# Kernel optimization log

Hardware: AMD Instinct MI355X
Metric: run time of the kernel (lower is better)

Reference implementation:

```python
import jax, jax.numpy as jnp
import numpy as np

N, E, K, F_IN, H = 50000, 640000, 3, 128, 128


def setup_inputs() -> dict:
    key = jax.random.key(0)
    ks = jax.random.split(key, 14)
    s = 0.05
    return {
        "x": jax.random.normal(ks[0], (N, F_IN), jnp.float32),
        "edge_index": jax.random.randint(ks[1], (2, E), 0, N, dtype=jnp.int32),
        "edge_weight": jax.random.uniform(ks[2], (E,), jnp.float32, minval=0.1, maxval=1.0),
        "W_x": jax.random.normal(ks[3], (4, F_IN, H), jnp.float32) * s,   # dense input weights (i,f,c,o)
        "w_c": jax.random.normal(ks[4], (3, H), jnp.float32) * s,         # peephole weights (i,f,o)
        "b": jax.random.normal(ks[5], (4, H), jnp.float32) * s,           # gate biases (i,f,c,o)
        "theta": jax.random.normal(ks[6], (4, K, H, H), jnp.float32) * s, # ChebConv weights per gate
        "theta_b": jax.random.normal(ks[7], (4, H), jnp.float32) * s,     # ChebConv biases per gate
        "gcn_w": jax.random.normal(ks[8], (H, H), jnp.float32) * s,
        "gcn_b": jnp.zeros((H,), jnp.float32),
        "bn_gamma": jnp.ones((H,), jnp.float32),
        "bn_beta": jnp.zeros((H,), jnp.float32),
        "bn_mean": jax.random.normal(ks[9], (H,), jnp.float32) * 0.1,
        "bn_var": jax.random.uniform(ks[10], (H,), jnp.float32, minval=0.5, maxval=1.5),
        "lin_w": jax.random.normal(ks[11], (H, 1), jnp.float32) * s,
        "lin_b": jnp.zeros((1,), jnp.float32),
    }


def reference(x, edge_index, edge_weight, W_x, w_c, b, theta, theta_b, gcn_w, gcn_b, bn_gamma, bn_beta, bn_mean, bn_var, lin_w, lin_b):
    n = x.shape[0]
    src, dst = edge_index[0], edge_index[1]

    # --- ChebConv normalization (sym, lambda_max=2): L_hat = -D^{-1/2} A D^{-1/2}, zero diagonal ---
    deg = jnp.zeros((n,), x.dtype).at[src].add(edge_weight)
    safe = jnp.where(deg > 0, deg, 1.0)
    dis = jnp.where(deg > 0, jax.lax.rsqrt(safe), 0.0)
    lw = -dis[src] * edge_weight * dis[dst]  # per-edge scaled-Laplacian weight

    def prop(h):  # out[i] = sum_{edges j->i} lw * h[j]
        return jnp.zeros_like(h).at[dst].add(lw[:, None] * h[src])

    def cheb(h, th, tb):  # sum_k T_k(L_hat) h @ theta_k + bias, Chebyshev recurrence
        Tx0, out = h, h @ th[0]
        Tx1 = prop(h)
        out = out + Tx1 @ th[1]
        for k in range(2, K):
            Tx2 = 2.0 * prop(Tx1) - Tx0
            out = out + Tx2 @ th[k]
            Tx0, Tx1 = Tx1, Tx2
        return out + tb

    # --- GCLSTM with H = C = 0 (module passes no initial state) ---
    Hs = jnp.zeros((n, W_x.shape[2]), x.dtype)
    Cs = jnp.zeros_like(Hs)
    I = jax.nn.sigmoid(x @ W_x[0] + cheb(Hs, theta[0], theta_b[0]) + w_c[0] * Cs + b[0])
    Fg = jax.nn.sigmoid(x @ W_x[1] + cheb(Hs, theta[1], theta_b[1]) + w_c[1] * Cs + b[1])
    T = jnp.tanh(x @ W_x[2] + cheb(Hs, theta[2], theta_b[2]) + b[2])
    Cs = Fg * Cs + I * T
    O = jax.nn.sigmoid(x @ W_x[3] + cheb(Hs, theta[3], theta_b[3]) + w_c[2] * Cs + b[3])
    Hs = O * jnp.tanh(Cs)

    # --- GCNConv(H) with unit edge weights + added self-loops ---
    h = Hs @ gcn_w
    deg_g = jnp.ones((n,), x.dtype).at[dst].add(jnp.ones((edge_index.shape[1],), x.dtype))
    dg = jax.lax.rsqrt(deg_g)
    g = jnp.zeros_like(h).at[dst].add((dg[src] * dg[dst])[:, None] * h[src]) + (dg * dg)[:, None] * h + gcn_b

    g = jax.nn.relu(g)
    g = bn_gamma * (g - bn_mean) * jax.lax.rsqrt(bn_var + 1e-5) + bn_beta  # BatchNorm1d (eval)
    return g @ lin_w + lin_b  # Dropout = identity in eval
```

## Files before the change

kernel.cpp:

```cpp
#include <hip/hip_runtime.h>
#include <hip/hip_bf16.h>

#define NN 50000
#define NE 640000
#define NP 196
#define CAP 64
#define NGB 782
#define NFB 625

typedef unsigned short ushort_t;
typedef unsigned int uint_t;
typedef __attribute__((ext_vector_type(8))) short bf16x8;
typedef __attribute__((ext_vector_type(4))) float f32x4;

__device__ __forceinline__ float b2f(ushort_t u) {
    union { uint_t u; float f; } v; v.u = ((uint_t)u) << 16; return v.f;
}
__device__ __forceinline__ ushort_t f2b(float f) {
    union { float f; uint_t u; } v; v.f = f;
    uint_t u = v.u;
    uint_t r = u + 0x7fffu + ((u >> 16) & 1u);
    return (ushort_t)(r >> 16);
}
__device__ __forceinline__ float fsig(float x)  { return __builtin_amdgcn_rcpf(1.0f + __expf(-x)); }
__device__ __forceinline__ float ftanh(float x) { return 1.0f - 2.0f * __builtin_amdgcn_rcpf(1.0f + __expf(2.0f * x)); }
__device__ __forceinline__ float ldm(const void* p, int i, int mf) {
    return mf ? ((const float*)p)[i] : b2f(((const ushort_t*)p)[i]);
}

#define OFF_HB   0
#define OFF_BSRC 12800000
#define OFF_CNT  25600000
#define OFF_WT   25800000
#define OFF_COEF 25931072
#define OFF_MODE 25933640
#define WS_REQ   25933648

__global__ void fb_k(ushort_t* __restrict__ out, int n) {
    int i = blockIdx.x * blockDim.x + threadIdx.x;
    if (i < n) out[i] = 0;
}

__global__ void init_k(const ushort_t* __restrict__ x, int* __restrict__ cnt,
                       int* __restrict__ mode) {
    __shared__ int s[256];
    int b = blockIdx.x, t = threadIdx.x;
    if (b < NP) {
        int i = b * 256 + t;
        if (i < NN) cnt[i] = 0;
    } else {
        int bad = 0;
        for (int i = t; i < 4096; i += 256) {
            int e = (x[i] >> 7) & 0xFF;
            if (e >= 0xC0) bad++;
        }
        s[t] = bad; __syncthreads();
        for (int o = 128; o >= 1; o >>= 1) { if (t < o) s[t] += s[t + o]; __syncthreads(); }
        if (t == 0) mode[0] = (s[0] > 8) ? 1 : 0;
    }
}

__global__ void prep_k(const void* __restrict__ Wx, const void* __restrict__ gcnw,
                       const void* __restrict__ wc, const void* __restrict__ bb,
                       const void* __restrict__ thb,
                       const void* __restrict__ gam, const void* __restrict__ bet,
                       const void* __restrict__ mea, const void* __restrict__ var,
                       const void* __restrict__ linw, const void* __restrict__ linb,
                       const int* __restrict__ mode,
                       ushort_t* __restrict__ WT, float* __restrict__ coef) {
    __shared__ float red[128];
    int b = blockIdx.x, t = threadIdx.x;
    int mf = mode[0];
    if (b < 32) {
        int gid = b * 256 + t;
        int m  = gid >> 11;
        int u  = gid & 2047;
        int k  = u >> 4;
        int f0 = (u & 15) << 3;
        const int srcoff[4] = { 0, 2 * 16384, 3 * 16384, 0 };
        const void* S = (m == 3) ? gcnw : Wx;
        int sbase = srcoff[m] + k * 128 + f0;
        ushort_t vals[8];
        if (mf == 0) {
            bf16x8 v = *(const bf16x8*)((const ushort_t*)S + sbase);
            #pragma unroll
            for (int i = 0; i < 8; i++) vals[i] = (ushort_t)v[i];
        } else {
            const float* Sf = (const float*)S + sbase;
            #pragma unroll
            for (int i = 0; i < 8; i++) vals[i] = f2b(Sf[i]);
        }
        ushort_t* D = WT + m * 16384 + k;
        #pragma unroll
        for (int i = 0; i < 8; i++) D[(f0 + i) * 128] = vals[i];
    } else {
        if (t < 128) {
            float rs = rsqrtf(ldm(var, t, mf) + 1e-5f);
            float ga = ldm(gam, t, mf);
            float lw = ldm(linw, t, mf);
            coef[t]       = ldm(thb, t, mf)           + ldm(bb, t, mf);
            coef[128 + t] = ldm(thb, 2 * 128 + t, mf) + ldm(bb, 2 * 128 + t, mf);
            coef[256 + t] = ldm(thb, 3 * 128 + t, mf) + ldm(bb, 3 * 128 + t, mf);
            coef[384 + t] = ldm(wc, 2 * 128 + t, mf);
            coef[512 + t] = ga * rs * lw;
            red[t] = (ldm(bet, t, mf) - ldm(mea, t, mf) * ga * rs) * lw;
        }
        __syncthreads();
        for (int off = 64; off >= 1; off >>= 1) {
            if (t < off && t < 128) red[t] += red[t + off];
            __syncthreads();
        }
        if (t == 0) coef[640] = red[0] + ldm(linb, 0, mf);
    }
}

__launch_bounds__(256)
__global__ void gafi_k(const void* __restrict__ x, const ushort_t* __restrict__ WT,
                       const float* __restrict__ coef, const int* __restrict__ mode,
                       ushort_t* __restrict__ hb,
                       const int* __restrict__ ei, int* __restrict__ cnt,
                       int* __restrict__ bsrc) {
    __shared__ ushort_t tile[64 * 136];
    int per = blockIdx.x / 9, rem = blockIdx.x % 9;
    int t = threadIdx.x;

    if (rem >= 5) {
        int fb = per * 4 + (rem - 5);
        if (fb >= NFB) return;
        int tid = fb * 256 + t;
        int4 s4 = ((const int4*)ei)[tid];
        int4 d4 = ((const int4*)(ei + NE))[tid];
        int p0 = atomicAdd(&cnt[d4.x], 1);
        int p1 = atomicAdd(&cnt[d4.y], 1);
        int p2 = atomicAdd(&cnt[d4.z], 1);
        int p3 = atomicAdd(&cnt[d4.w], 1);
        if (p0 < CAP) bsrc[d4.x * CAP + p0] = s4.x;
        if (p1 < CAP) bsrc[d4.y * CAP + p1] = s4.y;
        if (p2 < CAP) bsrc[d4.z * CAP + p2] = s4.z;
        if (p3 < CAP) bsrc[d4.w * CAP + p3] = s4.w;
        return;
    }

    int gb = per * 5 + rem;
    if (gb >= NGB) return;
    int base = gb * 64;
    int mf = mode[0];

    for (int i = 0; i < 4; i++) {
        int idx = (i * 256 + t) * 8;
        int row = idx >> 7, col = idx & 127;
        int n = base + row;
        bf16x8 v;
        if (n >= NN) {
            v = (bf16x8)0;
        } else if (mf == 0) {
            v = *(const bf16x8*)((const ushort_t*)x + n * 128 + col);
        } else {
            const float* xf = (const float*)x + n * 128 + col;
            float4 lo = *(const float4*)xf;
            float4 hi = *(const float4*)(xf + 4);
            v[0] = (short)f2b(lo.x); v[1] = (short)f2b(lo.y);
            v[2] = (short)f2b(lo.z); v[3] = (short)f2b(lo.w);
            v[4] = (short)f2b(hi.x); v[5] = (short)f2b(hi.y);
            v[6] = (short)f2b(hi.z); v[7] = (short)f2b(hi.w);
        }
        *(bf16x8*)&tile[row * 136 + col] = v;
    }
    __syncthreads();

    int lane = t & 63, wave = t >> 6;
    int m = lane & 15, quad = lane >> 4;

    bf16x8 a[4][4];
    #pragma unroll
    for (int rt = 0; rt < 4; rt++)
        #pragma unroll
        for (int kt = 0; kt < 4; kt++)
            a[rt][kt] = *(const bf16x8*)&tile[(rt * 16 + m) * 136 + kt * 32 + quad * 8];
    __syncthreads();

    const ushort_t* WTi = WT;
    const ushort_t* WTc = WT + 16384;
    const ushort_t* WTo = WT + 2 * 16384;

    #pragma unroll
    for (int ft = 0; ft < 2; ft++) {
        int f = wave * 32 + ft * 16 + m;
        bf16x8 bi[4], bc[4], bo[4];
        #pragma unroll
        for (int kt = 0; kt < 4; kt++) {
            int off = f * 128 + kt * 32 + quad * 8;
            bi[kt] = *(const bf16x8*)(WTi + off);
            bc[kt] = *(const bf16x8*)(WTc + off);
            bo[kt] = *(const bf16x8*)(WTo + off);
        }
        float bi_f = coef[f], bc_f = coef[128 + f], bo_f = coef[256 + f], w2 = coef[384 + f];
        #pragma unroll
        for (int rt = 0; rt < 4; rt++) {
            f32x4 ai = {0,0,0,0}, ac = {0,0,0,0}, ao = {0,0,0,0};
            #pragma unroll
            for (int kt = 0; kt < 4; kt++) {
                ai = __builtin_amdgcn_mfma_f32_16x16x32_bf16(a[rt][kt], bi[kt], ai, 0, 0, 0);
                ac = __builtin_amdgcn_mfma_f32_16x16x32_bf16(a[rt][kt], bc[kt], ac, 0, 0, 0);
                ao = __builtin_amdgcn_mfma_f32_16x16x32_bf16(a[rt][kt], bo[kt], ao, 0, 0, 0);
            }
            #pragma unroll
            for (int r = 0; r < 4; r++) {
                float I  = fsig(ai[r] + bi_f);
                float T  = ftanh(ac[r] + bc_f);
                float Cs = I * T;
                float O  = fsig(ao[r] + w2 * Cs + bo_f);
                float Hs = O * ftanh(Cs);
                tile[(rt * 16 + quad * 4 + r) * 136 + f] = f2b(Hs);
            }
        }
    }
    __syncthreads();

    const ushort_t* WTg = WT + 3 * 16384;
    bf16x8 ah[4][4];
    #pragma unroll
    for (int rt = 0; rt < 4; rt++)
        #pragma unroll
        for (int kt = 0; kt < 4; kt++)
            ah[rt][kt] = *(const bf16x8*)&tile[(rt * 16 + m) * 136 + kt * 32 + quad * 8];

    #pragma unroll
    for (int ft = 0; ft < 2; ft++) {
        int f = wave * 32 + ft * 16 + m;
        bf16x8 bg[4];
        #pragma unroll
        for (int kt = 0; kt < 4; kt++)
            bg[kt] = *(const bf16x8*)(WTg + f * 128 + kt * 32 + quad * 8);
        #pragma unroll
        for (int rt = 0; rt < 4; rt++) {
            f32x4 acc = {0,0,0,0};
            #pragma unroll
            for (int kt = 0; kt < 4; kt++)
                acc = __builtin_amdgcn_mfma_f32_16x16x32_bf16(ah[rt][kt], bg[kt], acc, 0, 0, 0);
            #pragma unroll
            for (int r = 0; r < 4; r++) {
                int n = base + rt * 16 + quad * 4 + r;
                if (n < NN) hb[n * 128 + f] = f2b(acc[r]);
            }
        }
    }
}

__launch_bounds__(256)
__global__ void gat_out_k(const ushort_t* __restrict__ hb, const int* __restrict__ cnt,
                          const int* __restrict__ bsrc,
                          const void* __restrict__ gcnb, const float* __restrict__ coef,
                          const int* __restrict__ mode, void* __restrict__ out) {
    int wid  = (blockIdx.x * blockDim.x + threadIdx.x) >> 6;
    int lane = threadIdx.x & 63;
    if (wid >= NN) return;
    int half = lane >> 5, sl = lane & 31;
    int c = cnt[wid]; if (c < 0) c = 0;
    int deg = (c < CAP) ? c : CAP;
    const int* brow = bsrc + wid * CAP;

    float a0 = 0.0f, a1 = 0.0f, a2 = 0.0f, a3 = 0.0f;
    int s0 = brow[half];
    int s1 = brow[half + 2];
    for (int j = half; j < deg; j += 4) {
        int sn0 = brow[(j + 4) & (CAP - 1)];
        int sn1 = brow[(j + 6) & (CAP - 1)];
        {
            int cs = cnt[s0]; if (cs < 0) cs = 0;
            uint2 r = *(const uint2*)(hb + s0 * 128 + sl * 4);
            float w = rsqrtf(1.0f + (float)cs);
            a0 += w * b2f((ushort_t)(r.x & 0xffffu));
            a1 += w * b2f((ushort_t)(r.x >> 16));
            a2 += w * b2f((ushort_t)(r.y & 0xffffu));
            a3 += w * b2f((ushort_t)(r.y >> 16));
        }
        if (j + 2 < deg) {
            int cs = cnt[s1]; if (cs < 0) cs = 0;
            uint2 r = *(const uint2*)(hb + s1 * 128 + sl * 4);
            float w = rsqrtf(1.0f + (float)cs);
            a0 += w * b2f((ushort_t)(r.x & 0xffffu));
            a1 += w * b2f((ushort_t)(r.x >> 16));
            a2 += w * b2f((ushort_t)(r.y & 0xffffu));
            a3 += w * b2f((ushort_t)(r.y >> 16));
        }
        s0 = sn0; s1 = sn1;
    }
    float d = rsqrtf(1.0f + (float)c);
    if (half == 0) {
        uint2 r = *(const uint2*)(hb + wid * 128 + sl * 4);
        a0 += d * b2f((ushort_t)(r.x & 0xffffu));
        a1 += d * b2f((ushort_t)(r.x >> 16));
        a2 += d * b2f((ushort_t)(r.y & 0xffffu));
        a3 += d * b2f((ushort_t)(r.y >> 16));
    }
    a0 += __shfl_xor(a0, 32); a1 += __shfl_xor(a1, 32);
    a2 += __shfl_xor(a2, 32); a3 += __shfl_xor(a3, 32);
    int mf = mode[0];
    int fb = sl * 4;
    float g0 = d * a0 + ldm(gcnb, fb,     mf);
    float g1 = d * a1 + ldm(gcnb, fb + 1, mf);
    float g2 = d * a2 + ldm(gcnb, fb + 2, mf);
    float g3 = d * a3 + ldm(gcnb, fb + 3, mf);
    float v = fmaxf(g0, 0.0f) * coef[512 + fb]
            + fmaxf(g1, 0.0f) * coef[512 + fb + 1]
            + fmaxf(g2, 0.0f) * coef[512 + fb + 2]
            + fmaxf(g3, 0.0f) * coef[512 + fb + 3];
    #pragma unroll
    for (int o = 32; o >= 1; o >>= 1) v += __shfl_down(v, o);
    if (lane == 0) {
        float r = 0.5f * v + coef[640];
        if (mf) ((float*)out)[wid] = r;
        else    ((ushort_t*)out)[wid] = f2b(r);
    }
}

extern "C" void kernel_launch(void* const* d_in, const int* in_sizes, int n_in,
                              void* d_out, int out_size, void* d_ws, size_t ws_size,
                              hipStream_t stream) {
    if (ws_size < (size_t)WS_REQ) {
        fb_k<<<(out_size + 255) / 256, 256, 0, stream>>>((ushort_t*)d_out, out_size);
        return;
    }
    const void* x    = d_in[0];
    const int*  ei   = (const int*)d_in[1];
    const void* Wx   = d_in[3];
    const void* wc   = d_in[4];
    const void* bb   = d_in[5];
    const void* thb  = d_in[7];
    const void* gcnw = d_in[8];
    const void* gcnb = d_in[9];
    const void* gam  = d_in[10];
    const void* bet  = d_in[11];
    const void* mea  = d_in[12];
    const void* var  = d_in[13];
    const void* linw = d_in[14];
    const void* linb = d_in[15];

    char* ws = (char*)d_ws;
    ushort_t* hb   = (ushort_t*)(ws + OFF_HB);
    int*      bsrc = (int*)     (ws + OFF_BSRC);
    int*      cnt  = (int*)     (ws + OFF_CNT);
    ushort_t* WT   = (ushort_t*)(ws + OFF_WT);
    float*    coef = (float*)   (ws + OFF_COEF);
    int*      mode = (int*)     (ws + OFF_MODE);

    init_k<<<NP + 1, 256, 0, stream>>>((const ushort_t*)x, cnt, mode);
    prep_k<<<33, 256, 0, stream>>>(Wx, gcnw, wc, bb, thb, gam, bet, mea, var, linw, linb, mode, WT, coef);
    gafi_k<<<157 * 9, 256, 0, stream>>>(x, WT, coef, mode, hb, ei, cnt, bsrc);
    gat_out_k<<<(NN * 64 + 255) / 256, 256, 0, stream>>>(hb, cnt, bsrc, gcnb, coef, mode, d_out);
}
```

Baseline: 187.4 us.

## Pad degree counters to 64B stride and merge init into prep kernel

Each per-node counter now sits on its own 64-byte slot (index shifted by 4), so the atomic increments in the edge bucketing phase no longer contend on shared cache lines. The zero-init and dtype-detection kernel is folded into the prep kernel, which removes one launch; each prep block recomputes the mode locally. The trade-off is a 16x larger counter array and scattered, non-coalesced counter reads in the gather kernel (one line per read).

```diff
diff --git a/kernel.cpp b/kernel.cpp
--- a/kernel.cpp
+++ b/kernel.cpp
@@ -3,7 +3,7 @@
 
 #define NN 50000
 #define NE 640000
-#define NP 196
+#define NZB 196
 #define CAP 64
 #define NGB 782
 #define NFB 625
@@ -28,51 +28,49 @@
     return mf ? ((const float*)p)[i] : b2f(((const ushort_t*)p)[i]);
 }
 
+#define CSH 4
 #define OFF_HB   0
 #define OFF_BSRC 12800000
 #define OFF_CNT  25600000
-#define OFF_WT   25800000
-#define OFF_COEF 25931072
-#define OFF_MODE 25933640
-#define WS_REQ   25933648
+#define OFF_WT   28800000
+#define OFF_COEF 28931072
+#define OFF_MODE 28933636
+#define WS_REQ   28933640
 
 __global__ void fb_k(ushort_t* __restrict__ out, int n) {
     int i = blockIdx.x * blockDim.x + threadIdx.x;
     if (i < n) out[i] = 0;
 }
 
-__global__ void init_k(const ushort_t* __restrict__ x, int* __restrict__ cnt,
-                       int* __restrict__ mode) {
-    __shared__ int s[256];
-    int b = blockIdx.x, t = threadIdx.x;
-    if (b < NP) {
-        int i = b * 256 + t;
-        if (i < NN) cnt[i] = 0;
-    } else {
-        int bad = 0;
-        for (int i = t; i < 4096; i += 256) {
-            int e = (x[i] >> 7) & 0xFF;
-            if (e >= 0xC0) bad++;
-        }
-        s[t] = bad; __syncthreads();
-        for (int o = 128; o >= 1; o >>= 1) { if (t < o) s[t] += s[t + o]; __syncthreads(); }
-        if (t == 0) mode[0] = (s[0] > 8) ? 1 : 0;
-    }
-}
-
-__global__ void prep_k(const void* __restrict__ Wx, const void* __restrict__ gcnw,
+__global__ void prep_k(const ushort_t* __restrict__ x,
+                       const void* __restrict__ Wx, const void* __restrict__ gcnw,
                        const void* __restrict__ wc, const void* __restrict__ bb,
                        const void* __restrict__ thb,
                        const void* __restrict__ gam, const void* __restrict__ bet,
                        const void* __restrict__ mea, const void* __restrict__ var,
                        const void* __restrict__ linw, const void* __restrict__ linb,
-                       const int* __restrict__ mode,
-                       ushort_t* __restrict__ WT, float* __restrict__ coef) {
+                       ushort_t* __restrict__ WT, float* __restrict__ coef,
+                       int* __restrict__ cnt, int* __restrict__ mode) {
+    __shared__ int si[256];
     __shared__ float red[128];
     int b = blockIdx.x, t = threadIdx.x;
-    int mf = mode[0];
-    if (b < 32) {
-        int gid = b * 256 + t;
+    if (b < NZB) {
+        int i = b * 256 + t;
+        if (i < NN) cnt[i << CSH] = 0;
+        return;
+    }
+    int bad = 0;
+    for (int i = t; i < 4096; i += 256) {
+        int e = (x[i] >> 7) & 0xFF;
+        if (e >= 0xC0) bad++;
+    }
+    si[t] = bad; __syncthreads();
+    for (int o = 128; o >= 1; o >>= 1) { if (t < o) si[t] += si[t + o]; __syncthreads(); }
+    int mf = (si[0] > 8) ? 1 : 0;
+
+    int wb = b - NZB;
+    if (wb < 32) {
+        int gid = wb * 256 + t;
         int m  = gid >> 11;
         int u  = gid & 2047;
         int k  = u >> 4;
@@ -110,7 +108,10 @@
             if (t < off && t < 128) red[t] += red[t + off];
             __syncthreads();
         }
-        if (t == 0) coef[640] = red[0] + ldm(linb, 0, mf);
+        if (t == 0) {
+            coef[640] = red[0] + ldm(linb, 0, mf);
+            mode[0] = mf;
+        }
     }
 }
 
@@ -130,10 +131,10 @@
         int tid = fb * 256 + t;
         int4 s4 = ((const int4*)ei)[tid];
         int4 d4 = ((const int4*)(ei + NE))[tid];
-        int p0 = atomicAdd(&cnt[d4.x], 1);
-        int p1 = atomicAdd(&cnt[d4.y], 1);
-        int p2 = atomicAdd(&cnt[d4.z], 1);
-        int p3 = atomicAdd(&cnt[d4.w], 1);
+        int p0 = atomicAdd(&cnt[d4.x << CSH], 1);
+        int p1 = atomicAdd(&cnt[d4.y << CSH], 1);
+        int p2 = atomicAdd(&cnt[d4.z << CSH], 1);
+        int p3 = atomicAdd(&cnt[d4.w << CSH], 1);
         if (p0 < CAP) bsrc[d4.x * CAP + p0] = s4.x;
         if (p1 < CAP) bsrc[d4.y * CAP + p1] = s4.y;
         if (p2 < CAP) bsrc[d4.z * CAP + p2] = s4.z;
@@ -256,7 +257,7 @@
     int lane = threadIdx.x & 63;
     if (wid >= NN) return;
     int half = lane >> 5, sl = lane & 31;
-    int c = cnt[wid]; if (c < 0) c = 0;
+    int c = cnt[wid << CSH]; if (c < 0) c = 0;
     int deg = (c < CAP) ? c : CAP;
     const int* brow = bsrc + wid * CAP;
 
@@ -267,7 +268,7 @@
         int sn0 = brow[(j + 4) & (CAP - 1)];
         int sn1 = brow[(j + 6) & (CAP - 1)];
         {
-            int cs = cnt[s0]; if (cs < 0) cs = 0;
+            int cs = cnt[s0 << CSH]; if (cs < 0) cs = 0;
             uint2 r = *(const uint2*)(hb + s0 * 128 + sl * 4);
             float w = rsqrtf(1.0f + (float)cs);
             a0 += w * b2f((ushort_t)(r.x & 0xffffu));
@@ -276,7 +277,7 @@
             a3 += w * b2f((ushort_t)(r.y >> 16));
         }
         if (j + 2 < deg) {
-            int cs = cnt[s1]; if (cs < 0) cs = 0;
+            int cs = cnt[s1 << CSH]; if (cs < 0) cs = 0;
             uint2 r = *(const uint2*)(hb + s1 * 128 + sl * 4);
             float w = rsqrtf(1.0f + (float)cs);
             a0 += w * b2f((ushort_t)(r.x & 0xffffu));
@@ -345,8 +346,8 @@
     float*    coef = (float*)   (ws + OFF_COEF);
     int*      mode = (int*)     (ws + OFF_MODE);
 
-    init_k<<<NP + 1, 256, 0, stream>>>((const ushort_t*)x, cnt, mode);
-    prep_k<<<33, 256, 0, stream>>>(Wx, gcnw, wc, bb, thb, gam, bet, mea, var, linw, linb, mode, WT, coef);
+    prep_k<<<NZB + 33, 256, 0, stream>>>((const ushort_t*)x, Wx, gcnw, wc, bb, thb,
+                                         gam, bet, mea, var, linw, linb, WT, coef, cnt, mode);
     gafi_k<<<157 * 9, 256, 0, stream>>>(x, WT, coef, mode, hb, ei, cnt, bsrc);
     gat_out_k<<<(NN * 64 + 255) / 256, 256, 0, stream>>>(hb, cnt, bsrc, gcnb, coef, mode, d_out);
 }
```

Result: no change. 187.9 us (+0.3%).
